# Optimization experiments

Measured on AMD Instinct MI355X. Metric: run time of the kernel, lower is better.

The kernel has to match this reference:

```python
import jax, jax.numpy as jnp
import numpy as np

G, N, F = 16, 2048, 32          # graphs, nodes/graph, node feature width
E = 32768                        # edges per graph (avg degree 16)
INPUT_DIM = N * F                # 65536, matches reshape in original forward
H, L = 512, 64                   # VAE hidden width, latent dim
BN_EPS = 1e-5
NEG_SLOPE = 0.01                 # nn.LeakyReLU default


def setup_inputs() -> dict:
    key = jax.random.key(0)
    ks = jax.random.split(key, 18)
    f32 = jnp.float32
    inp = {
        "x": jax.random.normal(ks[0], (G, N, F), dtype=f32),
        "edge_index": jax.random.randint(ks[1], (G, 2, E), 0, N, dtype=jnp.int32),
        "eps": jax.random.normal(ks[2], (G, L), dtype=f32),
        # GCNConv weight + bias
        "W_gcn": jax.random.normal(ks[3], (F, F), dtype=f32) / np.sqrt(F),
        "b_gcn": jnp.zeros((F,), dtype=f32),
        # BatchNorm1d(num_features) affine params
        "bn_gamma": jnp.ones((F,), dtype=f32),
        "bn_beta": jnp.zeros((F,), dtype=f32),
        # VAE encoder trunk + mean / log_var heads
        "W_enc": jax.random.normal(ks[4], (INPUT_DIM, H), dtype=f32) / np.sqrt(INPUT_DIM),
        "b_enc": jnp.zeros((H,), dtype=f32),
        "W_mu": jax.random.normal(ks[5], (H, L), dtype=f32) / np.sqrt(H),
        "b_mu": jnp.zeros((L,), dtype=f32),
        "W_lv": jax.random.normal(ks[6], (H, L), dtype=f32) / np.sqrt(H),
        "b_lv": jnp.zeros((L,), dtype=f32),
        # VAE decoder
        "W_dec1": jax.random.normal(ks[7], (L, H), dtype=f32) / np.sqrt(L),
        "b_dec1": jnp.zeros((H,), dtype=f32),
        "W_dec2": jax.random.normal(ks[8], (H, INPUT_DIM), dtype=f32) / np.sqrt(H),
        "b_dec2": jnp.zeros((INPUT_DIM,), dtype=f32),
    }
    return inp


def _gcn_conv(xg, eig, W_gcn, b_gcn):
    # PyG GCNConv: add self-loops, symmetric normalization D^-1/2 A D^-1/2
    src, dst = eig[0], eig[1]
    loop = jnp.arange(N, dtype=src.dtype)
    src = jnp.concatenate([src, loop])
    dst = jnp.concatenate([dst, loop])
    deg = jax.ops.segment_sum(jnp.ones(src.shape, dtype=xg.dtype), dst, num_segments=N)
    dinv = jax.lax.rsqrt(deg)  # deg >= 1 due to self-loops
    xw = xg @ W_gcn                                  # [N, F]
    coef = dinv[src] * dinv[dst]                     # [E+N]
    msg = xw[src] * coef[:, None]                    # gather + scale
    return jax.ops.segment_sum(msg, dst, num_segments=N) + b_gcn  # scatter-add


def reference(x, edge_index, eps, W_gcn, b_gcn, bn_gamma, bn_beta,
              W_enc, b_enc, W_mu, b_mu, W_lv, b_lv,
              W_dec1, b_dec1, W_dec2, b_dec2):
    # convolute(): per-graph GCN conv -> BatchNorm1d (batch stats over that graph's
    # nodes) -> tanh -> dropout (identity in eval) -> concat. Vectorized via vmap.
    h = jax.vmap(_gcn_conv, in_axes=(0, 0, None, None))(x, edge_index, W_gcn, b_gcn)  # [G,N,F]
    mu_n = h.mean(axis=1, keepdims=True)
    var_n = h.var(axis=1, keepdims=True)  # biased variance, as torch BN uses in normalization
    h = (h - mu_n) * jax.lax.rsqrt(var_n + BN_EPS) * bn_gamma + bn_beta
    h = jnp.tanh(h)
    xs = h.reshape(G, INPUT_DIM)
    # VariationalExample forward
    henc = jax.nn.leaky_relu(xs @ W_enc + b_enc, NEG_SLOPE)   # [G, H]
    mean = henc @ W_mu + b_mu                                  # [G, L]
    log_var = henc @ W_lv + b_lv                               # [G, L]
    z = mean + jnp.exp(0.5 * log_var) * eps                    # reparameterize
    hd = jax.nn.leaky_relu(z @ W_dec1 + b_dec1, NEG_SLOPE)     # [G, H]
    x_hat = hd @ W_dec2 + b_dec2                               # [G, INPUT_DIM]
    return x_hat, mean, log_var
```

## Files before the change

kernel.cpp:

```cpp
#include <hip/hip_runtime.h>
#include <hip/hip_bf16.h>

#define NG 16
#define NN 2048
#define NF 32
#define NE 32768
#define IND 65536
#define HD 512
#define LD 64

typedef unsigned int u32;


__global__ void k_xwdeg(const float* __restrict__ x, const float* __restrict__ Wg,
                        float* __restrict__ xw, const int* __restrict__ ei,
                        u32* __restrict__ deg){
  __shared__ float ws[32][33];
  __shared__ float xsh[8][32];
  int t = threadIdx.x;
  int bid = blockIdx.x;
  if (bid < 4096){
    for (int i = t; i < 1024; i += 256) ws[i >> 5][i & 31] = Wg[i];
    int base = bid * 8;
    int r = t >> 5, f = t & 31;
    xsh[r][f] = x[(base + r) * 32 + f];
    __syncthreads();
    float acc = 0.f;
    #pragma unroll
    for (int k = 0; k < 32; ++k) acc += xsh[r][k] * ws[k][f];
    xw[(base + r) * 32 + f] = acc;
  } else {
    int idx = (bid - 4096) * 256 + t;
    int g = idx >> 15, e = idx & (NE - 1);
    int dst = ei[(g * 2 + 1) * NE + e];
    atomicAdd(&deg[g * NN + dst], 1u);
  }
}

__global__ void k_prefix(const u32* __restrict__ deg, u32* __restrict__ offs,
                         float* __restrict__ dinv, u32* __restrict__ cursor){
  int g = blockIdx.x, t = threadIdx.x;
  const u32* dg = deg + g * NN;
  u32 loc[8]; u32 s = 0;
  #pragma unroll
  for (int i = 0; i < 8; ++i){ loc[i] = s; s += dg[t * 8 + i]; }
  __shared__ u32 bs[256];
  bs[t] = s; __syncthreads();
  for (int d = 1; d < 256; d <<= 1){
    u32 v = (t >= d) ? bs[t - d] : 0u;
    __syncthreads();
    bs[t] += v;
    __syncthreads();
  }
  u32 base = bs[t] - s;
  #pragma unroll
  for (int i = 0; i < 8; ++i){
    int n = t * 8 + i;
    offs[g * NN + n] = g * NE + base + loc[i];
    dinv[g * NN + n] = rsqrtf((float)(dg[n] + 1u));
    cursor[g * NN + n] = 0u;
  }
}

__global__ void k_sortedges(const int* __restrict__ ei, const u32* __restrict__ offs,
                            u32* __restrict__ cursor, u32* __restrict__ sorted){
  int idx = blockIdx.x * 256 + threadIdx.x;
  int g = idx >> 15, e = idx & (NE - 1);
  int src = ei[g * 2 * NE + e];
  int dst = ei[(g * 2 + 1) * NE + e];
  u32 pos = atomicAdd(&cursor[g * NN + dst], 1u);
  sorted[offs[g * NN + dst] + pos] = (u32)src;
}

__global__ void k_gather(const u32* __restrict__ sorted, const u32* __restrict__ offs,
                         const u32* __restrict__ deg, const float* __restrict__ dinv,
                         const float* __restrict__ xw, const float* __restrict__ bg,
                         float* __restrict__ h){
  int tid = blockIdx.x * 256 + threadIdx.x;
  int q = tid & 7, n = (tid >> 3) & (NN - 1), g = tid >> 14;
  int gn = g * NN + n;
  u32 o0 = offs[gn];
  u32 cnt = deg[gn];
  float dn = dinv[gn];
  const float4* xw4 = (const float4*)xw;
  float4 acc = make_float4(0.f, 0.f, 0.f, 0.f);
  for (u32 e = 0; e < cnt; ++e){
    u32 src = sorted[o0 + e];
    float c = dinv[g * NN + src] * dn;
    float4 v = xw4[(size_t)(g * NN + src) * 8 + q];
    acc.x += c * v.x; acc.y += c * v.y; acc.z += c * v.z; acc.w += c * v.w;
  }
  float c2 = dn * dn;
  float4 v = xw4[(size_t)gn * 8 + q];
  float4 b = ((const float4*)bg)[q];
  acc.x += c2 * v.x + b.x; acc.y += c2 * v.y + b.y;
  acc.z += c2 * v.z + b.z; acc.w += c2 * v.w + b.w;
  ((float4*)h)[(size_t)gn * 8 + q] = acc;
}


__global__ void k_bnstat(const float* __restrict__ h, float* __restrict__ pstat){
  int g = blockIdx.x >> 3, s = blockIdx.x & 7;
  int t = threadIdx.x, f = t & 31, r = t >> 5;
  float s1 = 0.f, s2 = 0.f;
  for (int it = 0; it < 32; ++it){
    int n = s * 256 + it * 8 + r;
    float v = h[(size_t)(g * NN + n) * 32 + f];
    s1 += v; s2 += v * v;
  }
  __shared__ float l1[256], l2[256];
  l1[t] = s1; l2[t] = s2;
  __syncthreads();
  if (t < 32){
    float a = 0.f, b = 0.f;
    #pragma unroll
    for (int r2 = 0; r2 < 8; ++r2){ a += l1[r2 * 32 + t]; b += l2[r2 * 32 + t]; }
    pstat[((g * 8 + s) * 32 + t) * 2 + 0] = a;
    pstat[((g * 8 + s) * 32 + t) * 2 + 1] = b;
  }
}


__global__ __launch_bounds__(256) void k_gemvenc(const float* __restrict__ h,
    const float* __restrict__ pstat, const float* __restrict__ gamma,
    const float* __restrict__ beta, const float* __restrict__ B,
    float* __restrict__ part){
  __shared__ float ash[128 * 17];
  __shared__ float ssc[512], ssh[512];
  int t = threadIdx.x;
  int k0 = blockIdx.x * 128;
  for (int i = t; i < 512; i += 256){
    int g = i >> 5, f = i & 31;
    float s1 = 0.f, s2 = 0.f;
    #pragma unroll
    for (int s = 0; s < 8; ++s){
      s1 += pstat[((g * 8 + s) * 32 + f) * 2 + 0];
      s2 += pstat[((g * 8 + s) * 32 + f) * 2 + 1];
    }
    float mean = s1 * (1.f / NN);
    float var  = s2 * (1.f / NN) - mean * mean;
    float sc = gamma[f] * rsqrtf(var + 1e-5f);
    ssc[i] = sc;
    ssh[i] = beta[f] - mean * sc;
  }
  __syncthreads();
  for (int idx = t; idx < 2048; idx += 256){
    int i = idx & 127, g = idx >> 7;
    int f = i & 31;
    float v = h[(size_t)g * IND + k0 + i];
    ash[i * 17 + g] = tanhf(v * ssc[g * 32 + f] + ssh[g * 32 + f]);
  }
  __syncthreads();
  float acc[32];
  #pragma unroll
  for (int i = 0; i < 32; ++i) acc[i] = 0.f;
  const float2* bp = (const float2*)(B + (size_t)k0 * 512) + t;
  for (int kk = 0; kk < 128; kk += 8){
    float2 bv[8];
    #pragma unroll
    for (int u = 0; u < 8; ++u) bv[u] = bp[(size_t)(kk + u) * 256];
    #pragma unroll
    for (int u = 0; u < 8; ++u){
      const float* ap = &ash[(kk + u) * 17];
      #pragma unroll
      for (int m = 0; m < 16; ++m){
        acc[2*m]   += ap[m] * bv[u].x;
        acc[2*m+1] += ap[m] * bv[u].y;
      }
    }
  }
  float* pp = part + (size_t)blockIdx.x * 8192 + t * 2;
  #pragma unroll
  for (int m = 0; m < 16; ++m)
    *(float2*)(pp + (size_t)m * 512) = make_float2(acc[2*m], acc[2*m+1]);
}

__global__ void k_encred1(const float* __restrict__ part, float* __restrict__ p2){
  int idx = blockIdx.x * 256 + threadIdx.x;
  int out = idx & 8191, grp = idx >> 13;
  const float* p = part + (size_t)grp * 64 * 8192 + out;
  float s = 0.f;
  #pragma unroll 8
  for (int c = 0; c < 64; ++c) s += p[(size_t)c * 8192];
  p2[idx] = s;
}

__global__ __launch_bounds__(512) void k_headdec(const float* __restrict__ p2,
    const float* __restrict__ be,
    const float* __restrict__ Wmu, const float* __restrict__ bmu,
    const float* __restrict__ Wlv, const float* __restrict__ blv,
    const float* __restrict__ eps, const float* __restrict__ W1,
    const float* __restrict__ b1, float* __restrict__ hdT, float* __restrict__ outp){
  int g = blockIdx.x, t = threadIdx.x;
  __shared__ float hsh[512];
  __shared__ float zsh[64];
  float hv = be[t];
  #pragma unroll
  for (int grp = 0; grp < 8; ++grp) hv += p2[grp * 8192 + g * 512 + t];
  hv = hv > 0.f ? hv : 0.01f * hv;
  hsh[t] = hv;
  __syncthreads();
  int l = t >> 3, r = t & 7;
  float am = 0.f, av = 0.f;
  for (int k = r; k < 512; k += 8){
    float hh = hsh[k];
    am += hh * Wmu[k * 64 + l];
    av += hh * Wlv[k * 64 + l];
  }
  #pragma unroll
  for (int d = 1; d < 8; d <<= 1){
    am += __shfl_xor(am, d);
    av += __shfl_xor(av, d);
  }
  if (r == 0){
    float mean = am + bmu[l];
    float lv   = av + blv[l];
    float z = mean + expf(0.5f * lv) * eps[g * 64 + l];
    zsh[l] = z;
    outp[1048576 + g * 64 + l] = mean;
    outp[1049600 + g * 64 + l] = lv;
  }
  __syncthreads();
  float a = 0.f;
  #pragma unroll
  for (int k = 0; k < 64; ++k) a += zsh[k] * W1[k * 512 + t];
  a += b1[t];
  a = a > 0.f ? a : 0.01f * a;
  hdT[t * 16 + g] = a;
}


__global__ __launch_bounds__(256) void k_gemvdec(const float* __restrict__ A,
                          const float* __restrict__ B,
                          float* __restrict__ part){
  __shared__ float ash[128 * 16];
  int t = threadIdx.x;
  int ks = blockIdx.x & 3;
  int nb = blockIdx.x >> 2;
  for (int i = t; i < 2048; i += 256) ash[i] = A[ks * 2048 + i];
  __syncthreads();
  float acc[32];
  #pragma unroll
  for (int i = 0; i < 32; ++i) acc[i] = 0.f;
  const float2* bp = (const float2*)(B + (size_t)ks * 128 * 65536) + nb * 256 + t;
  for (int kk = 0; kk < 128; kk += 8){
    float2 bv[8];
    #pragma unroll
    for (int u = 0; u < 8; ++u) bv[u] = bp[(size_t)(kk + u) * 32768];
    #pragma unroll
    for (int u = 0; u < 8; ++u){
      const float* ap = &ash[(kk + u) * 16];
      #pragma unroll
      for (int m = 0; m < 16; ++m){
        acc[2*m]   += ap[m] * bv[u].x;
        acc[2*m+1] += ap[m] * bv[u].y;
      }
    }
  }
  float* pp = part + (size_t)ks * 1048576 + nb * 512 + t * 2;
  #pragma unroll
  for (int m = 0; m < 16; ++m)
    *(float2*)(pp + (size_t)m * 65536) = make_float2(acc[2*m], acc[2*m+1]);
}

__global__ void k_decred(const float4* __restrict__ part, const float4* __restrict__ b2,
                         float4* __restrict__ outp){
  int idx = blockIdx.x * 256 + threadIdx.x;
  float4 s = b2[idx & 16383];
  #pragma unroll
  for (int ks = 0; ks < 4; ++ks){
    float4 p = part[(size_t)ks * 262144 + idx];
    s.x += p.x; s.y += p.y; s.z += p.z; s.w += p.w;
  }
  outp[idx] = s;
}


extern "C" void kernel_launch(void* const* d_in, const int* in_sizes, int n_in,
                              void* d_out, int out_size, void* d_ws, size_t ws_size,
                              hipStream_t stream){
  const float* x     = (const float*)d_in[0];
  const int*   ei    = (const int*)d_in[1];
  const float* eps   = (const float*)d_in[2];
  const float* Wg    = (const float*)d_in[3];
  const float* bg    = (const float*)d_in[4];
  const float* gamma = (const float*)d_in[5];
  const float* beta  = (const float*)d_in[6];
  const float* Wenc  = (const float*)d_in[7];
  const float* benc  = (const float*)d_in[8];
  const float* Wmu   = (const float*)d_in[9];
  const float* bmu   = (const float*)d_in[10];
  const float* Wlv   = (const float*)d_in[11];
  const float* blv   = (const float*)d_in[12];
  const float* Wd1   = (const float*)d_in[13];
  const float* bd1   = (const float*)d_in[14];
  const float* Wd2   = (const float*)d_in[15];
  const float* bd2   = (const float*)d_in[16];
  float* outp = (float*)d_out;

  char* ws = (char*)d_ws;
  const size_t OFF_XW     = 0;
  const size_t OFF_H      = 4194304;
  const size_t OFF_DEG    = 8388608;
  const size_t OFF_DINV   = 8519680;
  const size_t OFF_CURSOR = 8650752;
  const size_t OFF_PSTAT  = 8781824;
  const size_t OFF_HDT    = 8847360;
  const size_t OFF_P2     = 8880128;
  const size_t OFF_PART   = 9142272;
  const size_t OFF_SORT   = OFF_PART;
  const size_t OFF_OFFS   = OFF_PART + 2097152;

  float* xw     = (float*)(ws + OFF_XW);
  float* h      = (float*)(ws + OFF_H);
  u32*   deg    = (u32*)  (ws + OFF_DEG);
  float* dinv   = (float*)(ws + OFF_DINV);
  u32*   cursor = (u32*)  (ws + OFF_CURSOR);
  float* pstat  = (float*)(ws + OFF_PSTAT);
  float* hdT    = (float*)(ws + OFF_HDT);
  float* p2     = (float*)(ws + OFF_P2);
  float* part   = (float*)(ws + OFF_PART);
  u32*   sorted = (u32*)  (ws + OFF_SORT);
  u32*   offs   = (u32*)  (ws + OFF_OFFS);

  hipMemsetAsync(ws + OFF_DEG, 0, 131072, stream);

  k_xwdeg    <<<6144, 256, 0, stream>>>(x, Wg, xw, ei, deg);
  k_prefix   <<<16,   256, 0, stream>>>(deg, offs, dinv, cursor);
  k_sortedges<<<2048, 256, 0, stream>>>(ei, offs, cursor, sorted);
  k_gather   <<<1024, 256, 0, stream>>>(sorted, offs, deg, dinv, xw, bg, h);
  k_bnstat   <<<128,  256, 0, stream>>>(h, pstat);

  k_gemvenc  <<<512, 256, 0, stream>>>(h, pstat, gamma, beta, Wenc, part);
  k_encred1  <<<256, 256, 0, stream>>>(part, p2);

  k_headdec  <<<16, 512, 0, stream>>>(p2, benc, Wmu, bmu, Wlv, blv, eps, Wd1, bd1, hdT, outp);

  k_gemvdec  <<<512, 256, 0, stream>>>(hdT, Wd2, part);
  k_decred   <<<1024, 256, 0, stream>>>((const float4*)part, (const float4*)bd2, (float4*)outp);
}
```

Measured before the change: 179.9 us.

## Fuse decoder split-K reduction and bias into GEMV via shared memory

The decoder GEMV used to write four split-K partial outputs to global memory, and a separate kernel summed them and added the bias. Now each block owns a column tile and all four K-quarters. Each wave handles one quarter, the partials are reduced in shared memory, and the block adds the bias and writes the output directly. This removes a kernel launch and roughly 16 MB of partial-sum global traffic, at the cost of loading the full 32 KB A into LDS per block and extra syncs.

```diff
diff --git a/kernel.cpp b/kernel.cpp
--- a/kernel.cpp
+++ b/kernel.cpp
@@ -232,24 +232,26 @@
 
 __global__ __launch_bounds__(256) void k_gemvdec(const float* __restrict__ A,
                           const float* __restrict__ B,
-                          float* __restrict__ part){
-  __shared__ float ash[128 * 16];
+                          const float* __restrict__ bias,
+                          float* __restrict__ outp){
+  __shared__ float ash[8192];
   int t = threadIdx.x;
-  int ks = blockIdx.x & 3;
-  int nb = blockIdx.x >> 2;
-  for (int i = t; i < 2048; i += 256) ash[i] = A[ks * 2048 + i];
-  __syncthreads();
+  int nt = blockIdx.x;
+  for (int i = t; i < 8192; i += 256) ash[i] = A[i];
+  __syncthreads();
+  int cp = t & 63;
+  int kq = t >> 6;
   float acc[32];
   #pragma unroll
   for (int i = 0; i < 32; ++i) acc[i] = 0.f;
-  const float2* bp = (const float2*)(B + (size_t)ks * 128 * 65536) + nb * 256 + t;
+  const float2* bp = (const float2*)B + (size_t)(kq * 128) * 32768 + nt * 64 + cp;
   for (int kk = 0; kk < 128; kk += 8){
     float2 bv[8];
     #pragma unroll
     for (int u = 0; u < 8; ++u) bv[u] = bp[(size_t)(kk + u) * 32768];
     #pragma unroll
     for (int u = 0; u < 8; ++u){
-      const float* ap = &ash[(kk + u) * 16];
+      const float* ap = &ash[(kq * 128 + kk + u) * 16];
       #pragma unroll
       for (int m = 0; m < 16; ++m){
         acc[2*m]   += ap[m] * bv[u].x;
@@ -257,22 +259,27 @@
       }
     }
   }
-  float* pp = part + (size_t)ks * 1048576 + nb * 512 + t * 2;
-  #pragma unroll
-  for (int m = 0; m < 16; ++m)
-    *(float2*)(pp + (size_t)m * 65536) = make_float2(acc[2*m], acc[2*m+1]);
-}
-
-__global__ void k_decred(const float4* __restrict__ part, const float4* __restrict__ b2,
-                         float4* __restrict__ outp){
-  int idx = blockIdx.x * 256 + threadIdx.x;
-  float4 s = b2[idx & 16383];
-  #pragma unroll
-  for (int ks = 0; ks < 4; ++ks){
-    float4 p = part[(size_t)ks * 262144 + idx];
-    s.x += p.x; s.y += p.y; s.z += p.z; s.w += p.w;
-  }
-  outp[idx] = s;
+  __syncthreads();
+  #pragma unroll
+  for (int m = 0; m < 16; ++m){
+    ash[kq * 2048 + (m * 2 + 0) * 64 + cp] = acc[2*m];
+    ash[kq * 2048 + (m * 2 + 1) * 64 + cp] = acc[2*m+1];
+  }
+  __syncthreads();
+  #pragma unroll
+  for (int jj = 0; jj < 4; ++jj){
+    int idx = t * 4 + jj;
+    int m = idx >> 6, c = idx & 63;
+    float sx = 0.f, sy = 0.f;
+    #pragma unroll
+    for (int q = 0; q < 4; ++q){
+      sx += ash[q * 2048 + (m * 2 + 0) * 64 + c];
+      sy += ash[q * 2048 + (m * 2 + 1) * 64 + c];
+    }
+    float2 bb = ((const float2*)bias)[nt * 64 + c];
+    *(float2*)(outp + (size_t)m * 65536 + nt * 128 + c * 2) =
+        make_float2(sx + bb.x, sy + bb.y);
+  }
 }
 
 
@@ -336,6 +343,5 @@
 
   k_headdec  <<<16, 512, 0, stream>>>(p2, benc, Wmu, bmu, Wlv, blv, eps, Wd1, bd1, hdT, outp);
 
-  k_gemvdec  <<<512, 256, 0, stream>>>(hdT, Wd2, part);
-  k_decred   <<<1024, 256, 0, stream>>>((const float4*)part, (const float4*)bd2, (float4*)outp);
-}
+  k_gemvdec  <<<512, 256, 0, stream>>>(hdT, Wd2, bd2, outp);
+}
```

Measured after the change: 178.7 us. About the same (-0.6%).
